# Optimization experiments

Hardware: AMD Instinct MI355X
Metric: run time of the kernel (lower is better)

## Reference

```python
import jax, jax.numpy as jnp
import numpy as np

B, L, D = 8, 2048, 1024


def _hippo(d, seed=0):
    # Author's 'hippo_matrix': Q @ diag(arctan(linspace(0, pi, d))) @ Q.T with Q orthogonal.
    rng = np.random.default_rng(seed)
    Q, _ = np.linalg.qr(rng.standard_normal((d, d)))
    Dm = np.diag(np.arctan(np.linspace(0.0, np.pi, d)))
    return (Q @ Dm @ Q.T).astype(np.float32)


def setup_inputs() -> dict:
    key = jax.random.key(0)
    k1, k2, k3, k4 = jax.random.split(key, 4)
    x = jax.random.normal(k1, (B, L, D), jnp.float32)
    A_w = jnp.asarray(_hippo(D))                                   # [D, D], spectral norm <= arctan(pi)
    C_w = jax.random.normal(k2, (D, D), jnp.float32) * (D ** -0.5)  # readout C
    # rc maps cat(x_t, y_{t-1}, y_container) (3D) -> D; small init keeps the
    # linear recurrence spectral radius < 1 so the 2048-step scan stays finite.
    rc_w = jax.random.normal(k3, (D, 3 * D), jnp.float32) * (0.2 / np.sqrt(3 * D))
    rc_b = jax.random.normal(k4, (D,), jnp.float32) * 0.02
    return {"x": x, "A_w": A_w, "C_w": C_w, "rc_w": rc_w, "rc_b": rc_b}


def reference(x, A_w, C_w, rc_w, rc_b):
    # y[0] = x[0]; y[t] = C @ A @ (rc_w @ cat(x[t], y[t-1], y[t-1]) + rc_b)
    # (prev output enters twice: once via the outer forward_step cat, once via
    #  the LinearRecurrentContainer's internal memory y).
    d = x.shape[-1]
    Wx = rc_w[:, :d]                          # acts on x_t
    Wy = rc_w[:, d:2 * d] + rc_w[:, 2 * d:]   # both copies of y_{t-1}
    M = C_w @ A_w                             # fused C∘A readout, [D, D]
    P = M @ Wx                                # input map
    Q = M @ Wy                                # recurrence map
    c = M @ rc_b                              # fused bias
    u = jnp.einsum('bld,ed->ble', x[:, 1:], P) + c  # driving terms for t >= 1, [B, L-1, D]
    y0 = x[:, 0]                              # parallel_scan copies the first input verbatim

    def step(y_prev, u_t):
        y = u_t + y_prev @ Q.T                # [B, D]
        return y, y

    _, ys = jax.lax.scan(step, y0, jnp.swapaxes(u, 0, 1))  # [L-1, B, D]
    return jnp.concatenate([y0[:, None, :], jnp.swapaxes(ys, 0, 1)], axis=1)  # [B, L, D]
```

## Files before the change

kernel.cpp:

```cpp
#include <hip/hip_runtime.h>

typedef unsigned short u16;
typedef unsigned int   u32;
typedef __attribute__((ext_vector_type(8))) short short8;
typedef __attribute__((ext_vector_type(4))) short short4v;
typedef __attribute__((ext_vector_type(4))) float f32x4;

struct SqJobs {
  const u16* a[4];
  const u16* b[4];
  u16* c[4];
  u16* ct[4];
};

__device__ __forceinline__ float bf2f(u16 v) {
  u32 x = ((u32)v) << 16;
  return __builtin_bit_cast(float, x);
}
__device__ __forceinline__ u16 f2bf(float f) {
  u32 x = __builtin_bit_cast(u32, f);
  x += 0x7FFFu + ((x >> 16) & 1u);
  return (u16)(x >> 16);
}
__device__ __forceinline__ void gload_lds16(const u16* g, u16* l) {
  __builtin_amdgcn_global_load_lds(
      (const __attribute__((address_space(1))) u32*)g,
      (__attribute__((address_space(3))) u32*)l, 16, 0, 0);
}

template <int BM, int BN, int ADT, int BDT, int EPI, int AMAP, int OMAP,
          int COUT, int TRW, int SQF>
__global__ __launch_bounds__(256) void gemm_nt(
    const void* __restrict__ Av, int lda, const void* __restrict__ Bv, int ldb,
    void* __restrict__ Cv, int ldc, int Mrows, int K,
    const float* __restrict__ zrowF, const u16* __restrict__ zrowB,
    const float* __restrict__ bias, const float* __restrict__ addf,
    float* __restrict__ Yout, u16* __restrict__ aux16, int jp1, int shoff,
    SqJobs jb) {
  constexpr int WM = BM / 2, WN = BN / 2;
  constexpr int MT = WM / 16, NTT = WN / 16;
  constexpr int AIn = ADT ? BM * 8 : BM * 4;
  constexpr int BIn = BDT ? BN * 8 : BN * 4;
  static_assert(AIn >= 256 && BIn >= 256, "tile too small for 256 threads");
  constexpr int AI = AIn / 256, BI = BIn / 256;
  constexpr int LA = BM * 32, LB = BN * 32;
  constexpr bool PIPE3 = (ADT == 0 && BDT == 0 && BM == 64 && BN == 64);
  constexpr int NBUF = PIPE3 ? 3 : 2;
  __shared__ u16 lA[NBUF * LA];
  __shared__ u16 lB[NBUF * LB];
  const int tid = threadIdx.x;
  const int lane = tid & 63, wid = tid >> 6;
  const int wm = wid & 1, wn = wid >> 1;
  const bool role = (SQF > 0) && ((int)blockIdx.x >= SQF);
  const int pi = role ? (((int)blockIdx.x - SQF) >> 4) : 0;
  const int bxe = role ? (((int)blockIdx.x - SQF) & 15) : (int)blockIdx.x;
  const int m0 = bxe * BM, n0 = blockIdx.y * BN;
  const int effM = role ? 1024 : Mrows;
  const int q = lane >> 4, lm = lane & 15;
  const int cq = (q ^ ((lm >> 1) & 3)) * 8;

  const u16* corrB = nullptr;
  if constexpr (EPI == 7)
    corrB = (blockIdx.z == 0)
                ? (const u16*)Bv
                : jb.a[0] + (long)((int)blockIdx.z - 1) * 1048576;

  f32x4 acc[MT][NTT];
#pragma unroll
  for (int mi = 0; mi < MT; ++mi)
#pragma unroll
    for (int ni = 0; ni < NTT; ++ni) acc[mi][ni] = (f32x4){0.f, 0.f, 0.f, 0.f};

  const u16* aB[AI];
  const float* aF[AI];
#pragma unroll
  for (int i = 0; i < AI; ++i) {
    int g = tid + i * 256;
    int r = ADT ? (g >> 3) : (g >> 2);
    int c = ADT ? (g & 7) : (g & 3);
    int row = m0 + r;
    bool valid = (row < effM);
    if (AMAP == 1 && !role) {
      int p = row % 257;
      if (p < shoff) valid = false;
      row -= shoff;
    }
    if constexpr (ADT == 1) {
      int cs = ((((c >> 1) ^ ((r >> 1) & 3)) << 1) | (c & 1)) * 4;
      aF[i] = (valid ? (const float*)Av + (long)row * lda : zrowF) + cs;
    } else {
      int cs = (c ^ ((r >> 1) & 3)) * 8;
      const u16* base;
      if (role)
        base = jb.a[pi] + (long)row * 1024;
      else
        base = valid ? (const u16*)Av + (long)row * lda : zrowB;
      aB[i] = base + cs;
    }
  }
  const u16* bB[BI];
  const float* bF[BI];
#pragma unroll
  for (int i = 0; i < BI; ++i) {
    int g = tid + i * 256;
    int r = BDT ? (g >> 3) : (g >> 2);
    int c = BDT ? (g & 7) : (g & 3);
    if constexpr (BDT == 1) {
      int cs = ((((c >> 1) ^ ((r >> 1) & 3)) << 1) | (c & 1)) * 4;
      bF[i] = (const float*)Bv + (long)(n0 + r) * ldb + cs;
    } else {
      int cs = (c ^ ((r >> 1) & 3)) * 8;
      const u16* base;
      if (role) {
        base = jb.b[pi] + (long)(n0 + r) * 1024;
      } else {
        if constexpr (EPI == 7)
          base = corrB + (long)(n0 + r) * ldb;
        else
          base = (const u16*)Bv + (long)(n0 + r) * ldb;
      }
      bB[i] = base + cs;
    }
  }

  if constexpr (PIPE3) {
    static_assert(AI == 1 && BI == 1, "PIPE3 assumes 1+1 issues/thread");
    gload_lds16(aB[0], &lA[tid * 8]);
    gload_lds16(bB[0], &lB[tid * 8]);
    gload_lds16(aB[0] + 32, &lA[LA + tid * 8]);
    gload_lds16(bB[0] + 32, &lB[LB + tid * 8]);
    const int NS = K >> 5;
    int cb = 0, pb = 2;
    for (int ks = 0; ks < NS; ++ks) {
      __builtin_amdgcn_sched_barrier(0);
      if (ks + 1 < NS)
        asm volatile("s_waitcnt vmcnt(2)" ::: "memory");
      else
        asm volatile("s_waitcnt vmcnt(0)" ::: "memory");
      __builtin_amdgcn_s_barrier();
      __builtin_amdgcn_sched_barrier(0);
      if (ks + 2 < NS) {
        const int kp = (ks + 2) << 5;
        gload_lds16(aB[0] + kp, &lA[pb * LA + tid * 8]);
        gload_lds16(bB[0] + kp, &lB[pb * LB + tid * 8]);
      }
      const int ca = cb * LA, cbb = cb * LB;
      short8 af[MT], bfr[NTT];
#pragma unroll
      for (int mi = 0; mi < MT; ++mi)
        af[mi] = *(const short8*)&lA[ca + (wm * WM + mi * 16 + lm) * 32 + cq];
#pragma unroll
      for (int ni = 0; ni < NTT; ++ni)
        bfr[ni] =
            *(const short8*)&lB[cbb + (wn * WN + ni * 16 + lm) * 32 + cq];
#pragma unroll
      for (int mi = 0; mi < MT; ++mi)
#pragma unroll
        for (int ni = 0; ni < NTT; ++ni)
          acc[mi][ni] = __builtin_amdgcn_mfma_f32_16x16x32_bf16(
              af[mi], bfr[ni], acc[mi][ni], 0, 0, 0);
      cb = (cb == 2) ? 0 : cb + 1;
      pb = (pb == 2) ? 0 : pb + 1;
    }
  } else {
    if constexpr (ADT == 1) {
      f32x4 f0[AI];
#pragma unroll
      for (int i = 0; i < AI; ++i) f0[i] = *(const f32x4*)(aF[i]);
#pragma unroll
      for (int i = 0; i < AI; ++i) {
        short4v s = {(short)f2bf(f0[i][0]), (short)f2bf(f0[i][1]),
                     (short)f2bf(f0[i][2]), (short)f2bf(f0[i][3])};
        *(short4v*)&lA[(tid + i * 256) * 4] = s;
      }
    } else {
#pragma unroll
      for (int i = 0; i < AI; ++i)
        gload_lds16(aB[i], &lA[(tid + i * 256) * 8]);
    }
    if constexpr (BDT == 1) {
      f32x4 f0[BI];
#pragma unroll
      for (int i = 0; i < BI; ++i) f0[i] = *(const f32x4*)(bF[i]);
#pragma unroll
      for (int i = 0; i < BI; ++i) {
        short4v s = {(short)f2bf(f0[i][0]), (short)f2bf(f0[i][1]),
                     (short)f2bf(f0[i][2]), (short)f2bf(f0[i][3])};
        *(short4v*)&lB[(tid + i * 256) * 4] = s;
      }
    } else {
#pragma unroll
      for (int i = 0; i < BI; ++i)
        gload_lds16(bB[i], &lB[(tid + i * 256) * 8]);
    }
    __syncthreads();

    int cur = 0;
    for (int k0 = 0; k0 < K; k0 += 32) {
      const int kn = k0 + 32;
      const bool more = kn < K;
      const int nxA = (cur ^ 1) * LA, nxB = (cur ^ 1) * LB;
      f32x4 fa[AI], fb[BI];
      if (more) {
        if constexpr (ADT == 1) {
#pragma unroll
          for (int i = 0; i < AI; ++i) fa[i] = *(const f32x4*)(aF[i] + kn);
        } else {
#pragma unroll
          for (int i = 0; i < AI; ++i)
            gload_lds16(aB[i] + kn, &lA[nxA + (tid + i * 256) * 8]);
        }
        if constexpr (BDT == 1) {
#pragma unroll
          for (int i = 0; i < BI; ++i) fb[i] = *(const f32x4*)(bF[i] + kn);
        } else {
#pragma unroll
          for (int i = 0; i < BI; ++i)
            gload_lds16(bB[i] + kn, &lB[nxB + (tid + i * 256) * 8]);
        }
      }
      short8 af[MT], bf[NTT];
#pragma unroll
      for (int mi = 0; mi < MT; ++mi)
        af[mi] =
            *(const short8*)&lA[cur * LA + (wm * WM + mi * 16 + lm) * 32 + cq];
#pragma unroll
      for (int ni = 0; ni < NTT; ++ni)
        bf[ni] =
            *(const short8*)&lB[cur * LB + (wn * WN + ni * 16 + lm) * 32 + cq];
#pragma unroll
      for (int mi = 0; mi < MT; ++mi)
#pragma unroll
        for (int ni = 0; ni < NTT; ++ni)
          acc[mi][ni] = __builtin_amdgcn_mfma_f32_16x16x32_bf16(
              af[mi], bf[ni], acc[mi][ni], 0, 0, 0);
      if (more) {
        if constexpr (ADT == 1) {
#pragma unroll
          for (int i = 0; i < AI; ++i) {
            short4v s = {(short)f2bf(fa[i][0]), (short)f2bf(fa[i][1]),
                         (short)f2bf(fa[i][2]), (short)f2bf(fa[i][3])};
            *(short4v*)&lA[nxA + (tid + i * 256) * 4] = s;
          }
        }
        if constexpr (BDT == 1) {
#pragma unroll
          for (int i = 0; i < BI; ++i) {
            short4v s = {(short)f2bf(fb[i][0]), (short)f2bf(fb[i][1]),
                         (short)f2bf(fb[i][2]), (short)f2bf(fb[i][3])};
            *(short4v*)&lB[nxB + (tid + i * 256) * 4] = s;
          }
        }
      }
      __syncthreads();
      cur ^= 1;
    }
  }

#pragma unroll
  for (int mi = 0; mi < MT; ++mi) {
    int rbase = m0 + wm * WM + mi * 16 + q * 4;
#pragma unroll
    for (int ni = 0; ni < NTT; ++ni) {
      int ocol = n0 + wn * WN + ni * 16 + lm;
#pragma unroll
      for (int r = 0; r < 4; ++r) {
        int orow = rbase + r;
        float v = acc[mi][ni][r];
        if (role) {
          if (orow < 1024) {
            u16 ov = f2bf(v);
            jb.c[pi][(long)orow * 1024 + ocol] = ov;
            if (jb.ct[pi]) jb.ct[pi][(long)ocol * 1024 + orow] = ov;
          }
          continue;
        }
        if (orow >= Mrows) continue;
        if constexpr (EPI == 7) {
          long urow = 8L * orow + ((int)blockIdx.z + 1);
          float vv = v + addf[urow * 1024 + ocol];
          Yout[urow * 1024 + ocol] = vv;
          continue;
        }
        if constexpr (EPI == 5) {
          v += bias[ocol];
          bool isT0 = (orow & 2047) == 0;
          if (isT0) v = addf[(long)orow * 1024 + ocol];
          ((float*)Cv)[(long)orow * ldc + ocol] = v;
          if (isT0) Yout[((long)(orow >> 11) * 257) * 1024 + ocol] = v;
          if ((orow & 7) == 1)
            aux16[((long)(orow >> 3)) * 1024 + ocol] = f2bf(v);
          continue;
        }
        if constexpr (EPI == 6) {
          v += addf[(long)orow * 1024 + ocol];
          ((float*)Cv)[(long)orow * ldc + ocol] = v;
          int b = orow / 257;
          int pp_ = orow - b * 257;
          if (pp_ < 256)
            aux16[((long)(b * 256 + pp_)) * 1024 + ocol] = f2bf(v);
          if (pp_ >= 1 && pp_ < 256)
            Yout[((long)b * 2048 + 8L * pp_) * 1024 + ocol] = v;
          continue;
        }
        long urow = 0;
        bool uok = true;
        if constexpr (EPI == 2 || EPI == 3) {
          urow = 8L * orow + jp1;
          uok = ((urow & 2047) != 0);
          if (uok) v += addf[urow * 1024 + ocol];
        }
        if constexpr (EPI == 4) v += addf[(long)orow * 1024 + ocol];
        long wrow = orow;
        if constexpr (OMAP == 1)
          wrow = (long)(orow >> 8) * 257 + (orow & 255) + 1;
        if constexpr (COUT == 1)
          ((float*)Cv)[wrow * (long)ldc + ocol] = v;
        else
          ((u16*)Cv)[wrow * (long)ldc + ocol] = f2bf(v);
        if constexpr (TRW == 1) aux16[(long)ocol * ldc + orow] = f2bf(v);
        if constexpr (EPI == 3) {
          if (uok) Yout[urow * 1024 + ocol] = v;
        }
      }
    }
  }
}

__global__ void zero_misc(float* zF, u16* zB) {
  for (int i = threadIdx.x; i < 2048; i += 256) {
    zF[i] = 0.f;
    zB[i] = 0;
  }
}
__global__ void xconv(const float* __restrict__ x, u16* __restrict__ xb) {
  long i = (long)blockIdx.x * 256 + threadIdx.x;
  f32x4 v = ((const f32x4*)x)[i];
  short4v s = {(short)f2bf(v[0]), (short)f2bf(v[1]), (short)f2bf(v[2]),
               (short)f2bf(v[3])};
  ((short4v*)xb)[i] = s;
}
__global__ void prep_wt(const float* __restrict__ rc_w, u16* __restrict__ WxT,
                        u16* __restrict__ WyT) {
  __shared__ u16 tx[64][65];
  __shared__ u16 ty[64][65];
  int kb = blockIdx.x * 64, db = blockIdx.y * 64;
  for (int i = threadIdx.x; i < 64 * 64; i += 256) {
    int r = i >> 6, c = i & 63;
    long base = (long)(kb + r) * 3072 + db + c;
    tx[r][c] = f2bf(rc_w[base]);
    ty[r][c] = f2bf(rc_w[base + 1024] + rc_w[base + 2048]);
  }
  __syncthreads();
  for (int i = threadIdx.x; i < 64 * 64; i += 256) {
    int r = i >> 6, c = i & 63;
    WxT[(long)(db + r) * 1024 + kb + c] = tx[c][r];
    WyT[(long)(db + r) * 1024 + kb + c] = ty[c][r];
  }
}
__global__ void matvec_c(const u16* __restrict__ M_,
                         const float* __restrict__ rb,
                         float* __restrict__ cvec) {
  int row = blockIdx.x;
  int lane = threadIdx.x;
  float s = 0.f;
  for (int k = lane; k < 1024; k += 64)
    s += bf2f(M_[(long)row * 1024 + k]) * rb[k];
  for (int o = 32; o > 0; o >>= 1) s += __shfl_down(s, o, 64);
  if (lane == 0) cvec[row] = s;
}

extern "C" void kernel_launch(void* const* d_in, const int* in_sizes, int n_in,
                              void* d_out, int out_size, void* d_ws,
                              size_t ws_size, hipStream_t stream) {
  const float* x = (const float*)d_in[0];
  const float* A_w = (const float*)d_in[1];
  const float* C_w = (const float*)d_in[2];
  const float* rc_w = (const float*)d_in[3];
  const float* rc_b = (const float*)d_in[4];
  float* Y = (float*)d_out;

  char* ws = (char*)d_ws;
  const long MB = 1 << 20;
  u16* Z0 = (u16*)(ws);
  u16* Z1 = (u16*)(ws + 4 * MB);
  float* Bnd0 = (float*)(ws + 8 * MB);
  float* Bnd1 = (float*)(ws + 8 * MB + 8912896);
  char* p = ws + 25 * MB;
  u16* Mbuf = (u16*)p;
  u16* WxT = (u16*)(p + 2 * MB);
  u16* WyT = (u16*)(p + 4 * MB);
  u16* Pbuf = (u16*)(p + 6 * MB);
  u16* Qbuf = (u16*)(p + 8 * MB);
  u16* QbufT = (u16*)(p + 10 * MB);
  float* cvec = (float*)(p + 12 * MB);
  float* zF = (float*)(p + 12 * MB + 4096);
  u16* zB = (u16*)(p + 12 * MB + 12288);
  u16* xbf = (u16*)(p + 12 * MB + 16384);
  const size_t need_fast = (size_t)(25 * MB + 12 * MB + 16384) + 33554432;
  const bool fast = ws_size >= need_fast;

  SqJobs J0{};
  dim3 blk(256);
  zero_misc<<<dim3(1), blk, 0, stream>>>(zF, zB);
  if (fast) xconv<<<dim3(16384), blk, 0, stream>>>(x, xbf);
  prep_wt<<<dim3(16, 16), blk, 0, stream>>>(rc_w, WxT, WyT);

  gemm_nt<64, 64, 1, 1, 0, 0, 0, 0, 0, 0><<<dim3(16, 16), blk, 0, stream>>>(
      C_w, 1024, A_w, 1024, Mbuf, 1024, 1024, 1024, zF, zB, nullptr, nullptr,
      nullptr, nullptr, 0, 0, J0);
  SqJobs sjPQ{};
  sjPQ.a[0] = Mbuf;
  sjPQ.b[0] = WxT;
  sjPQ.c[0] = Pbuf;
  gemm_nt<64, 64, 0, 0, 0, 0, 0, 0, 1, 16><<<dim3(32, 16), blk, 0, stream>>>(
      Mbuf, 1024, WyT, 1024, Qbuf, 1024, 1024, 1024, zF, zB, nullptr, nullptr,
      nullptr, QbufT, 0, 0, sjPQ);
  matvec_c<<<dim3(1024), dim3(64), 0, stream>>>(Mbuf, rc_b, cvec);

  if (fast)
    gemm_nt<128, 128, 0, 0, 5, 0, 0, 1, 0, 0>
        <<<dim3(128, 8), blk, 0, stream>>>(xbf, 1024, Pbuf, 1024, Y, 1024,
                                           16384, 1024, zF, zB, cvec, x, Bnd0,
                                           Z0, 0, 0, J0);
  else
    gemm_nt<128, 128, 1, 0, 5, 0, 0, 1, 0, 0>
        <<<dim3(128, 8), blk, 0, stream>>>(x, 1024, Pbuf, 1024, Y, 1024, 16384,
                                           1024, zF, zB, cvec, x, Bnd0, Z0, 0,
                                           0, J0);

  if (fast) {
    const long M1 = 1048576;
    u16* PW = xbf;
    u16* Tb2 = xbf + 6 * M1;
    u16* Tt2 = xbf + 7 * M1;
    u16* Tb3 = xbf + 8 * M1;
    u16* Tt3 = xbf + 9 * M1;
    u16* Tb4 = xbf + 10 * M1;
    u16* Tt4 = xbf + 11 * M1;
    u16* Tb5 = xbf + 12 * M1;
    u16* Tt5 = xbf + 13 * M1;
    u16* Tb6 = xbf + 14 * M1;
    u16* Tt6 = xbf + 15 * M1;
    u16* Tt0 = Mbuf;
    u16* Tt1 = WxT;
    u16* Pw3T = WyT;

    SqJobs sj[7] = {};
    int nsq[7] = {1, 2, 4, 1, 1, 1, 1};
    sj[0].a[0] = Qbuf;        sj[0].b[0] = QbufT; sj[0].c[0] = PW;          sj[0].ct[0] = Tt0;
    sj[1].a[0] = PW;          sj[1].b[0] = Tt0;   sj[1].c[0] = PW + 2 * M1; sj[1].ct[0] = Tt1;
    sj[1].a[1] = PW;          sj[1].b[1] = QbufT; sj[1].c[1] = PW + 1 * M1; sj[1].ct[1] = Pw3T;
    sj[2].a[0] = PW + 2 * M1; sj[2].b[0] = Tt1;   sj[2].c[0] = Tb2;         sj[2].ct[0] = Tt2;
    sj[2].a[1] = PW + 2 * M1; sj[2].b[1] = QbufT; sj[2].c[1] = PW + 3 * M1;
    sj[2].a[2] = PW + 2 * M1; sj[2].b[2] = Tt0;   sj[2].c[2] = PW + 4 * M1;
    sj[2].a[3] = PW + 2 * M1; sj[2].b[3] = Pw3T;  sj[2].c[3] = PW + 5 * M1;
    sj[3].a[0] = Tb2;         sj[3].b[0] = Tt2;   sj[3].c[0] = Tb3;         sj[3].ct[0] = Tt3;
    sj[4].a[0] = Tb3;         sj[4].b[0] = Tt3;   sj[4].c[0] = Tb4;         sj[4].ct[0] = Tt4;
    sj[5].a[0] = Tb4;         sj[5].b[0] = Tt4;   sj[5].c[0] = Tb5;         sj[5].ct[0] = Tt5;
    sj[6].a[0] = Tb5;         sj[6].b[0] = Tt5;   sj[6].c[0] = Tb6;         sj[6].ct[0] = Tt6;

    for (int j = 1; j <= 6; ++j) {
      const u16* zin = (j & 1) ? Z0 : Z1;
      u16* zout = (j & 1) ? Z1 : Z0;
      gemm_nt<64, 64, 0, 0, 3, 0, 0, 0, 0, 32>
          <<<dim3(32 + 16 * nsq[j - 1], 16), blk, 0, stream>>>(
              zin, 1024, Qbuf, 1024, zout, 1024, 2048, 1024, zF, zB, nullptr,
              Y, Y, nullptr, j + 1, 0, sj[j - 1]);
    }
    gemm_nt<64, 64, 0, 0, 2, 0, 1, 1, 0, 32><<<dim3(48, 16), blk, 0, stream>>>(
        Z0, 1024, Qbuf, 1024, Bnd0, 1024, 2048, 1024, zF, zB, nullptr, Y,
        nullptr, nullptr, 8, 0, sj[6]);

    u16* TbP2[5] = {Tb2, Tb3, Tb4, Tb5, Tb6};
    float* bc = Bnd0;
    float* bn = Bnd1;
    for (int s = 0; s < 5; ++s) {
      if (s < 4)
        gemm_nt<64, 64, 1, 0, 4, 1, 0, 1, 0, 0>
            <<<dim3(33, 16), blk, 0, stream>>>(bc, 1024, TbP2[s], 1024, bn,
                                               1024, 2056, 1024, zF, zB,
                                               nullptr, bc, nullptr, nullptr,
                                               0, 1 << s, J0);
      else
        gemm_nt<64, 64, 1, 0, 6, 1, 0, 1, 0, 0>
            <<<dim3(33, 16), blk, 0, stream>>>(bc, 1024, TbP2[s], 1024, bn,
                                               1024, 2056, 1024, zF, zB,
                                               nullptr, bc, Y, Z0, 0, 1 << s,
                                               J0);
      float* t = bc;
      bc = bn;
      bn = t;
    }

    SqJobs cj{};
    cj.a[0] = PW;
    gemm_nt<64, 64, 0, 0, 7, 0, 0, 0, 0, 0>
        <<<dim3(32, 16, 7), blk, 0, stream>>>(Z0, 1024, Qbuf, 1024, Z1, 1024,
                                              2048, 1024, zF, zB, nullptr, Y,
                                              Y, nullptr, 0, 0, cj);
  } else {
    u16* Tb[7];
    u16* Tt[7];
    for (int i = 0; i < 7; ++i) {
      Tb[i] = (i & 1) ? Mbuf : WxT;
      Tt[i] = (i & 1) ? Pbuf : WyT;
    }
    for (int j = 1; j <= 6; ++j) {
      const u16* zin = (j & 1) ? Z0 : Z1;
      u16* zout = (j & 1) ? Z1 : Z0;
      gemm_nt<64, 64, 0, 0, 2, 0, 0, 0, 0, 0>
          <<<dim3(32, 16), blk, 0, stream>>>(zin, 1024, Qbuf, 1024, zout, 1024,
                                             2048, 1024, zF, zB, nullptr, Y,
                                             nullptr, nullptr, j + 1, 0, J0);
    }
    gemm_nt<64, 64, 0, 0, 2, 0, 1, 1, 0, 0><<<dim3(32, 16), blk, 0, stream>>>(
        Z0, 1024, Qbuf, 1024, Bnd0, 1024, 2048, 1024, zF, zB, nullptr, Y,
        nullptr, nullptr, 8, 0, J0);
    for (int i = 0; i < 3; ++i) {
      const u16* si = (i == 0) ? Qbuf : Tb[i - 1];
      const u16* st = (i == 0) ? QbufT : Tt[i - 1];
      gemm_nt<64, 64, 0, 0, 0, 0, 0, 0, 1, 0>
          <<<dim3(16, 16), blk, 0, stream>>>(si, 1024, st, 1024, Tb[i], 1024,
                                             1024, 1024, zF, zB, nullptr,
                                             nullptr, nullptr, Tt[i], 0, 0,
                                             J0);
    }
    float* bc = Bnd0;
    float* bn = Bnd1;
    for (int s = 0; s < 5; ++s) {
      if (s < 4)
        gemm_nt<64, 64, 1, 0, 4, 1, 0, 1, 0, 0>
            <<<dim3(33, 16), blk, 0, stream>>>(bc, 1024, Tb[s + 2], 1024, bn,
                                               1024, 2056, 1024, zF, zB,
                                               nullptr, bc, nullptr, nullptr,
                                               0, 1 << s, J0);
      else
        gemm_nt<64, 64, 1, 0, 6, 1, 0, 1, 0, 0>
            <<<dim3(33, 16), blk, 0, stream>>>(bc, 1024, Tb[s + 2], 1024, bn,
                                               1024, 2056, 1024, zF, zB,
                                               nullptr, bc, Y, Z0, 0, 1 << s,
                                               J0);
      if (s < 4) {
        int i = s + 3;
        gemm_nt<64, 64, 0, 0, 0, 0, 0, 0, 1, 0>
            <<<dim3(16, 16), blk, 0, stream>>>(Tb[i - 1], 1024, Tt[i - 1],
                                               1024, Tb[i], 1024, 1024, 1024,
                                               zF, zB, nullptr, nullptr,
                                               nullptr, Tt[i], 0, 0, J0);
      }
      float* t = bc;
      bc = bn;
      bn = t;
    }
    for (int j = 0; j <= 7; ++j) {
      const u16* zin = (j & 1) ? Z1 : Z0;
      u16* zout = (j & 1) ? Z0 : Z1;
      gemm_nt<64, 64, 0, 0, 3, 0, 0, 0, 0, 0>
          <<<dim3(32, 16), blk, 0, stream>>>(zin, 1024, Qbuf, 1024, zout, 1024,
                                             2048, 1024, zF, zB, nullptr, Y, Y,
                                             nullptr, j + 1, 0, J0);
    }
  }
}
```

Before: 643.5 us.

## Fold small prep kernels into GEMM launches and remap final GEMM blocks across XCDs

Three standalone launches are removed by folding their work into existing kernels. The zero-fill now runs inside prep_wt, the x-to-bf16 conversion runs in extra blocks of the M=C·A GEMM, and the bias matvec runs in extra blocks of the P/Q GEMM. This cuts launch overhead and lets the small jobs overlap with GEMM work. The final multi-plane correction GEMM also remaps its linear block index so that each of seven XCDs handles one z-plane, which should improve L2 reuse of each plane's B matrix. The cost is heavier kernel templates and imbalanced blocks sharing a grid.

```diff
diff --git a/kernel.cpp b/kernel.cpp
--- a/kernel.cpp
+++ b/kernel.cpp
@@ -29,7 +29,7 @@
 }
 
 template <int BM, int BN, int ADT, int BDT, int EPI, int AMAP, int OMAP,
-          int COUT, int TRW, int SQF>
+          int COUT, int TRW, int SQF, int XTRA>
 __global__ __launch_bounds__(256) void gemm_nt(
     const void* __restrict__ Av, int lda, const void* __restrict__ Bv, int ldb,
     void* __restrict__ Cv, int ldc, int Mrows, int K,
@@ -37,6 +37,38 @@
     const float* __restrict__ bias, const float* __restrict__ addf,
     float* __restrict__ Yout, u16* __restrict__ aux16, int jp1, int shoff,
     SqJobs jb) {
+  if constexpr (XTRA == 1) {
+    if ((int)blockIdx.x >= 16) {
+      const f32x4* xs = (const f32x4*)jb.a[3];
+      short4v* xd = (short4v*)jb.c[3];
+      const long id = ((long)blockIdx.x - 16) * 16 + blockIdx.y;
+      const long base = id * 4096 + threadIdx.x;
+#pragma unroll
+      for (int k = 0; k < 16; ++k) {
+        f32x4 v = xs[base + k * 256];
+        short4v s = {(short)f2bf(v[0]), (short)f2bf(v[1]), (short)f2bf(v[2]),
+                     (short)f2bf(v[3])};
+        xd[base + k * 256] = s;
+      }
+      return;
+    }
+  }
+  if constexpr (XTRA == 2) {
+    if ((int)blockIdx.x >= 32) {
+      const u16* Mb = (const u16*)Av;
+      const float* rb = (const float*)jb.b[3];
+      float* cv = (float*)jb.ct[3];
+      int row = (((int)blockIdx.x - 32) * 16 + (int)blockIdx.y) * 4 +
+                ((int)threadIdx.x >> 6);
+      int ln = threadIdx.x & 63;
+      float s = 0.f;
+      for (int k = ln; k < 1024; k += 64)
+        s += bf2f(Mb[(long)row * 1024 + k]) * rb[k];
+      for (int o = 32; o > 0; o >>= 1) s += __shfl_down(s, o, 64);
+      if (ln == 0) cv[row] = s;
+      return;
+    }
+  }
   constexpr int WM = BM / 2, WN = BN / 2;
   constexpr int MT = WM / 16, NTT = WN / 16;
   constexpr int AIn = ADT ? BM * 8 : BM * 4;
@@ -54,16 +86,29 @@
   const bool role = (SQF > 0) && ((int)blockIdx.x >= SQF);
   const int pi = role ? (((int)blockIdx.x - SQF) >> 4) : 0;
   const int bxe = role ? (((int)blockIdx.x - SQF) & 15) : (int)blockIdx.x;
-  const int m0 = bxe * BM, n0 = blockIdx.y * BN;
+  int m0 = bxe * BM, n0 = blockIdx.y * BN;
+  int zpl = (int)blockIdx.z;
+  if constexpr (EPI == 7) {
+    int lin = (int)blockIdx.x + 32 * (int)blockIdx.y + 512 * (int)blockIdx.z;
+    int xcd = lin & 7, loc = lin >> 3;
+    int t;
+    if (xcd < 7) {
+      zpl = xcd;
+      t = loc;
+    } else {
+      zpl = loc >> 6;
+      t = 448 + (loc & 63);
+    }
+    m0 = (t >> 4) * 64;
+    n0 = (t & 15) * 64;
+  }
   const int effM = role ? 1024 : Mrows;
   const int q = lane >> 4, lm = lane & 15;
   const int cq = (q ^ ((lm >> 1) & 3)) * 8;
 
   const u16* corrB = nullptr;
   if constexpr (EPI == 7)
-    corrB = (blockIdx.z == 0)
-                ? (const u16*)Bv
-                : jb.a[0] + (long)((int)blockIdx.z - 1) * 1048576;
+    corrB = (zpl == 0) ? (const u16*)Bv : jb.a[0] + (long)(zpl - 1) * 1048576;
 
   f32x4 acc[MT][NTT];
 #pragma unroll
@@ -277,7 +322,7 @@
         }
         if (orow >= Mrows) continue;
         if constexpr (EPI == 7) {
-          long urow = 8L * orow + ((int)blockIdx.z + 1);
+          long urow = 8L * orow + (zpl + 1);
           float vv = v + addf[urow * 1024 + ocol];
           Yout[urow * 1024 + ocol] = vv;
           continue;
@@ -327,23 +372,16 @@
   }
 }
 
-__global__ void zero_misc(float* zF, u16* zB) {
-  for (int i = threadIdx.x; i < 2048; i += 256) {
-    zF[i] = 0.f;
-    zB[i] = 0;
-  }
-}
-__global__ void xconv(const float* __restrict__ x, u16* __restrict__ xb) {
-  long i = (long)blockIdx.x * 256 + threadIdx.x;
-  f32x4 v = ((const f32x4*)x)[i];
-  short4v s = {(short)f2bf(v[0]), (short)f2bf(v[1]), (short)f2bf(v[2]),
-               (short)f2bf(v[3])};
-  ((short4v*)xb)[i] = s;
-}
 __global__ void prep_wt(const float* __restrict__ rc_w, u16* __restrict__ WxT,
-                        u16* __restrict__ WyT) {
+                        u16* __restrict__ WyT, float* zF, u16* zB) {
   __shared__ u16 tx[64][65];
   __shared__ u16 ty[64][65];
+  if (blockIdx.x == 0 && blockIdx.y == 0) {
+    for (int i = threadIdx.x; i < 2048; i += 256) {
+      zF[i] = 0.f;
+      zB[i] = 0;
+    }
+  }
   int kb = blockIdx.x * 64, db = blockIdx.y * 64;
   for (int i = threadIdx.x; i < 64 * 64; i += 256) {
     int r = i >> 6, c = i & 63;
@@ -357,17 +395,6 @@
     WxT[(long)(db + r) * 1024 + kb + c] = tx[c][r];
     WyT[(long)(db + r) * 1024 + kb + c] = ty[c][r];
   }
-}
-__global__ void matvec_c(const u16* __restrict__ M_,
-                         const float* __restrict__ rb,
-                         float* __restrict__ cvec) {
-  int row = blockIdx.x;
-  int lane = threadIdx.x;
-  float s = 0.f;
-  for (int k = lane; k < 1024; k += 64)
-    s += bf2f(M_[(long)row * 1024 + k]) * rb[k];
-  for (int o = 32; o > 0; o >>= 1) s += __shfl_down(s, o, 64);
-  if (lane == 0) cvec[row] = s;
 }
 
 extern "C" void kernel_launch(void* const* d_in, const int* in_sizes, int n_in,
@@ -402,29 +429,33 @@
 
   SqJobs J0{};
   dim3 blk(256);
-  zero_misc<<<dim3(1), blk, 0, stream>>>(zF, zB);
-  if (fast) xconv<<<dim3(16384), blk, 0, stream>>>(x, xbf);
-  prep_wt<<<dim3(16, 16), blk, 0, stream>>>(rc_w, WxT, WyT);
-
-  gemm_nt<64, 64, 1, 1, 0, 0, 0, 0, 0, 0><<<dim3(16, 16), blk, 0, stream>>>(
-      C_w, 1024, A_w, 1024, Mbuf, 1024, 1024, 1024, zF, zB, nullptr, nullptr,
-      nullptr, nullptr, 0, 0, J0);
+  prep_wt<<<dim3(16, 16), blk, 0, stream>>>(rc_w, WxT, WyT, zF, zB);
+
+  SqJobs sjM{};
+  sjM.a[3] = (const u16*)x;
+  sjM.c[3] = (u16*)xbf;
+  gemm_nt<64, 64, 1, 1, 0, 0, 0, 0, 0, 0, 1>
+      <<<dim3(fast ? 80 : 16, 16), blk, 0, stream>>>(
+          C_w, 1024, A_w, 1024, Mbuf, 1024, 1024, 1024, zF, zB, nullptr,
+          nullptr, nullptr, nullptr, 0, 0, sjM);
   SqJobs sjPQ{};
   sjPQ.a[0] = Mbuf;
   sjPQ.b[0] = WxT;
   sjPQ.c[0] = Pbuf;
-  gemm_nt<64, 64, 0, 0, 0, 0, 0, 0, 1, 16><<<dim3(32, 16), blk, 0, stream>>>(
-      Mbuf, 1024, WyT, 1024, Qbuf, 1024, 1024, 1024, zF, zB, nullptr, nullptr,
-      nullptr, QbufT, 0, 0, sjPQ);
-  matvec_c<<<dim3(1024), dim3(64), 0, stream>>>(Mbuf, rc_b, cvec);
+  sjPQ.b[3] = (const u16*)rc_b;
+  sjPQ.ct[3] = (u16*)cvec;
+  gemm_nt<64, 64, 0, 0, 0, 0, 0, 0, 1, 16, 2>
+      <<<dim3(48, 16), blk, 0, stream>>>(Mbuf, 1024, WyT, 1024, Qbuf, 1024,
+                                         1024, 1024, zF, zB, nullptr, nullptr,
+                                         nullptr, QbufT, 0, 0, sjPQ);
 
   if (fast)
-    gemm_nt<128, 128, 0, 0, 5, 0, 0, 1, 0, 0>
+    gemm_nt<128, 128, 0, 0, 5, 0, 0, 1, 0, 0, 0>
         <<<dim3(128, 8), blk, 0, stream>>>(xbf, 1024, Pbuf, 1024, Y, 1024,
                                            16384, 1024, zF, zB, cvec, x, Bnd0,
                                            Z0, 0, 0, J0);
   else
-    gemm_nt<128, 128, 1, 0, 5, 0, 0, 1, 0, 0>
+    gemm_nt<128, 128, 1, 0, 5, 0, 0, 1, 0, 0, 0>
         <<<dim3(128, 8), blk, 0, stream>>>(x, 1024, Pbuf, 1024, Y, 1024, 16384,
                                            1024, zF, zB, cvec, x, Bnd0, Z0, 0,
                                            0, J0);
@@ -463,27 +494,28 @@
     for (int j = 1; j <= 6; ++j) {
       const u16* zin = (j & 1) ? Z0 : Z1;
       u16* zout = (j & 1) ? Z1 : Z0;
-      gemm_nt<64, 64, 0, 0, 3, 0, 0, 0, 0, 32>
+      gemm_nt<64, 64, 0, 0, 3, 0, 0, 0, 0, 32, 0>
           <<<dim3(32 + 16 * nsq[j - 1], 16), blk, 0, stream>>>(
               zin, 1024, Qbuf, 1024, zout, 1024, 2048, 1024, zF, zB, nullptr,
               Y, Y, nullptr, j + 1, 0, sj[j - 1]);
     }
-    gemm_nt<64, 64, 0, 0, 2, 0, 1, 1, 0, 32><<<dim3(48, 16), blk, 0, stream>>>(
-        Z0, 1024, Qbuf, 1024, Bnd0, 1024, 2048, 1024, zF, zB, nullptr, Y,
-        nullptr, nullptr, 8, 0, sj[6]);
+    gemm_nt<64, 64, 0, 0, 2, 0, 1, 1, 0, 32, 0>
+        <<<dim3(48, 16), blk, 0, stream>>>(Z0, 1024, Qbuf, 1024, Bnd0, 1024,
+                                           2048, 1024, zF, zB, nullptr, Y,
+                                           nullptr, nullptr, 8, 0, sj[6]);
 
     u16* TbP2[5] = {Tb2, Tb3, Tb4, Tb5, Tb6};
     float* bc = Bnd0;
     float* bn = Bnd1;
     for (int s = 0; s < 5; ++s) {
       if (s < 4)
-        gemm_nt<64, 64, 1, 0, 4, 1, 0, 1, 0, 0>
+        gemm_nt<64, 64, 1, 0, 4, 1, 0, 1, 0, 0, 0>
             <<<dim3(33, 16), blk, 0, stream>>>(bc, 1024, TbP2[s], 1024, bn,
                                                1024, 2056, 1024, zF, zB,
                                                nullptr, bc, nullptr, nullptr,
                                                0, 1 << s, J0);
       else
-        gemm_nt<64, 64, 1, 0, 6, 1, 0, 1, 0, 0>
+        gemm_nt<64, 64, 1, 0, 6, 1, 0, 1, 0, 0, 0>
             <<<dim3(33, 16), blk, 0, stream>>>(bc, 1024, TbP2[s], 1024, bn,
                                                1024, 2056, 1024, zF, zB,
                                                nullptr, bc, Y, Z0, 0, 1 << s,
@@ -495,7 +527,7 @@
 
     SqJobs cj{};
     cj.a[0] = PW;
-    gemm_nt<64, 64, 0, 0, 7, 0, 0, 0, 0, 0>
+    gemm_nt<64, 64, 0, 0, 7, 0, 0, 0, 0, 0, 0>
         <<<dim3(32, 16, 7), blk, 0, stream>>>(Z0, 1024, Qbuf, 1024, Z1, 1024,
                                               2048, 1024, zF, zB, nullptr, Y,
                                               Y, nullptr, 0, 0, cj);
@@ -509,18 +541,19 @@
     for (int j = 1; j <= 6; ++j) {
       const u16* zin = (j & 1) ? Z0 : Z1;
       u16* zout = (j & 1) ? Z1 : Z0;
-      gemm_nt<64, 64, 0, 0, 2, 0, 0, 0, 0, 0>
+      gemm_nt<64, 64, 0, 0, 2, 0, 0, 0, 0, 0, 0>
           <<<dim3(32, 16), blk, 0, stream>>>(zin, 1024, Qbuf, 1024, zout, 1024,
                                              2048, 1024, zF, zB, nullptr, Y,
                                              nullptr, nullptr, j + 1, 0, J0);
     }
-    gemm_nt<64, 64, 0, 0, 2, 0, 1, 1, 0, 0><<<dim3(32, 16), blk, 0, stream>>>(
-        Z0, 1024, Qbuf, 1024, Bnd0, 1024, 2048, 1024, zF, zB, nullptr, Y,
-        nullptr, nullptr, 8, 0, J0);
+    gemm_nt<64, 64, 0, 0, 2, 0, 1, 1, 0, 0, 0>
+        <<<dim3(32, 16), blk, 0, stream>>>(Z0, 1024, Qbuf, 1024, Bnd0, 1024,
+                                           2048, 1024, zF, zB, nullptr, Y,
+                                           nullptr, nullptr, 8, 0, J0);
     for (int i = 0; i < 3; ++i) {
       const u16* si = (i == 0) ? Qbuf : Tb[i - 1];
       const u16* st = (i == 0) ? QbufT : Tt[i - 1];
-      gemm_nt<64, 64, 0, 0, 0, 0, 0, 0, 1, 0>
+      gemm_nt<64, 64, 0, 0, 0, 0, 0, 0, 1, 0, 0>
           <<<dim3(16, 16), blk, 0, stream>>>(si, 1024, st, 1024, Tb[i], 1024,
                                              1024, 1024, zF, zB, nullptr,
                                              nullptr, nullptr, Tt[i], 0, 0,
@@ -530,20 +563,20 @@
     float* bn = Bnd1;
     for (int s = 0; s < 5; ++s) {
       if (s < 4)
-        gemm_nt<64, 64, 1, 0, 4, 1, 0, 1, 0, 0>
+        gemm_nt<64, 64, 1, 0, 4, 1, 0, 1, 0, 0, 0>
             <<<dim3(33, 16), blk, 0, stream>>>(bc, 1024, Tb[s + 2], 1024, bn,
                                                1024, 2056, 1024, zF, zB,
                                                nullptr, bc, nullptr, nullptr,
                                                0, 1 << s, J0);
       else
-        gemm_nt<64, 64, 1, 0, 6, 1, 0, 1, 0, 0>
+        gemm_nt<64, 64, 1, 0, 6, 1, 0, 1, 0, 0, 0>
             <<<dim3(33, 16), blk, 0, stream>>>(bc, 1024, Tb[s + 2], 1024, bn,
                                                1024, 2056, 1024, zF, zB,
                                                nullptr, bc, Y, Z0, 0, 1 << s,
                                                J0);
       if (s < 4) {
         int i = s + 3;
-        gemm_nt<64, 64, 0, 0, 0, 0, 0, 0, 1, 0>
+        gemm_nt<64, 64, 0, 0, 0, 0, 0, 0, 1, 0, 0>
             <<<dim3(16, 16), blk, 0, stream>>>(Tb[i - 1], 1024, Tt[i - 1],
                                                1024, Tb[i], 1024, 1024, 1024,
                                                zF, zB, nullptr, nullptr,
@@ -556,7 +589,7 @@
     for (int j = 0; j <= 7; ++j) {
       const u16* zin = (j & 1) ? Z1 : Z0;
       u16* zout = (j & 1) ? Z0 : Z1;
-      gemm_nt<64, 64, 0, 0, 3, 0, 0, 0, 0, 0>
+      gemm_nt<64, 64, 0, 0, 3, 0, 0, 0, 0, 0, 0>
           <<<dim3(32, 16), blk, 0, stream>>>(zin, 1024, Qbuf, 1024, zout, 1024,
                                              2048, 1024, zF, zB, nullptr, Y, Y,
                                              nullptr, j + 1, 0, J0);
```

New measurement: 626.5 us. 2.6% less time.
